# Optimization experiments

Measured on AMD Instinct MI355X. Metric: run time of the kernel, lower is better.

The kernel has to match this reference:

```python
import jax, jax.numpy as jnp
import numpy as np

B, T, C = 128, 512, 128  # batch, seq_len, num_tags


def setup_inputs() -> dict:
    key = jax.random.key(0)
    k1, k2, k3 = jax.random.split(key, 3)
    labels = jax.random.randint(k1, (B, T), 0, C)
    y_true = jax.nn.one_hot(labels, C, dtype=jnp.float32)  # dense one-hot targets
    y_pred = jax.random.normal(k2, (B, T, C), dtype=jnp.float32)  # emission scores
    mask = jnp.ones((B, T), dtype=jnp.float32)
    # glorot_uniform for (C,C): limit = sqrt(6/(C+C))
    limit = np.sqrt(6.0 / (C + C)).astype(np.float32)
    trans = jax.random.uniform(k3, (C, C), dtype=jnp.float32, minval=-limit, maxval=limit)
    return {"y_true": y_true, "y_pred": y_pred, "mask": mask, "trans": trans}


def reference(y_true, y_pred, mask, trans):
    # Faithful translation of ConditionalRandomField.dense_loss (lr_multiplier=1).
    m = mask[..., None]                      # (B,T,1)
    y_true = y_true * m
    y_pred = y_pred * m
    # real path score
    emission = jnp.einsum('bnc,bnc->b', y_true, y_pred)
    transition = jnp.einsum('bni,ij,bnj->b', y_true[:, :-1], trans, y_true[:, 1:])
    real_path_score = emission + transition  # (B,)
    # forward algorithm: sequential logsumexp recurrence (K.rnn equivalent)
    init = y_pred[:, 0]                      # (B,C)
    xs = (jnp.swapaxes(y_pred[:, 1:], 0, 1),  # (T-1,B,C)
          jnp.swapaxes(mask[:, 1:], 0, 1))    # (T-1,B)

    def step(state, xm):
        x_t, m_t = xm
        # state: (B,C) alpha; trans: (C,C)
        new = jax.nn.logsumexp(state[:, :, None] + trans[None, :, :], axis=1) + x_t
        state = jnp.where(m_t[:, None] > 0, new, state)  # masked steps carry prev state
        return state, None

    last, _ = jax.lax.scan(step, init, xs)
    all_paths_score = jax.nn.logsumexp(last, axis=1)  # (B,)
    return all_paths_score - real_path_score          # (B,) per-sample CRF NLL
```

## Files before the change

kernel.cpp:

```cpp
#include <hip/hip_runtime.h>

#define BB 128
#define TT 512
#define CC 128

typedef short short8 __attribute__((ext_vector_type(8)));
typedef float f32x4  __attribute__((ext_vector_type(4)));
typedef unsigned u32x4 __attribute__((ext_vector_type(4)));

__device__ __forceinline__ unsigned pk_trunc(float a, float b) {
    return __builtin_amdgcn_perm(__float_as_uint(a), __float_as_uint(b), 0x03020706u);
}
__device__ __forceinline__ unsigned short f2bf(float f) {
    unsigned u = __float_as_uint(f);
    u += 0x7fffu + ((u >> 16) & 1u);
    return (unsigned short)(u >> 16);
}
__device__ __forceinline__ float lo16f(unsigned u) { return __uint_as_float(u << 16); }
__device__ __forceinline__ float hi16f(unsigned u) { return __uint_as_float(u & 0xffff0000u); }

#define MFMA16(A, B, C) __builtin_amdgcn_mfma_f32_16x16x32_bf16((A), (B), (C), 0, 0, 0)

#define DOSTEP(AP_, P_, RPAR_, TN_) do {                                       \
    const unsigned* sb = &sbuf[RPAR_][0];                                      \
    unsigned* sw = &sbuf[(RPAR_) ^ 1][0];                                      \
    u32x4 Rv1 = *(const u32x4*)(sb + rd1);                                     \
    u32x4 Rv2 = *(const u32x4*)(sb + rd2);                                     \
    u32x4 Rv3 = *(const u32x4*)(sb + rd3);                                     \
    unsigned bcu = 0;                                                          \
    if (AP_) bcu = sb[bcaddr];                    \
    const float mm = pfm[P_];                                                  \
    float e0[4], e1[4];                                                        \
    e0[0] = __expf(pfa[P_].x * mm); e0[1] = __expf(pfa[P_].y * mm);            \
    e0[2] = __expf(pfa[P_].z * mm); e0[3] = __expf(pfa[P_].w * mm);            \
    e1[0] = __expf(pfb[P_].x * mm); e1[1] = __expf(pfb[P_].y * mm);            \
    e1[2] = __expf(pfb[P_].z * mm); e1[3] = __expf(pfb[P_].w * mm);            \
    union { u32x4 u; short8 s; } cO, c1, c2, c3;                               \
    cO.u[0] = BfO[0]; cO.u[1] = BfO[1]; cO.u[2] = BfO[2]; cO.u[3] = BfO[3];    \
    c1.u = Rv1; c2.u = Rv2; c3.u = Rv3;                                        \
    f32x4 aA0 = {0.f,0.f,0.f,0.f}, aA1 = {0.f,0.f,0.f,0.f};                    \
    f32x4 aB0 = {0.f,0.f,0.f,0.f}, aB1 = {0.f,0.f,0.f,0.f};                    \
    aA0 = MFMA16(AfP[0][0], cO.s, aA0);  aA1 = MFMA16(AfP[1][0], cO.s, aA1);   \
    aA0 = MFMA16(AfP[0][1], c1.s, aA0);  aA1 = MFMA16(AfP[1][1], c1.s, aA1);   \
    aB0 = MFMA16(AfP[0][2], c2.s, aB0);  aB1 = MFMA16(AfP[1][2], c2.s, aB1);   \
    aB0 = MFMA16(AfP[0][3], c3.s, aB0);  aB1 = MFMA16(AfP[1][3], c3.s, aB1);   \
    f32x4 ac0 = aA0 + aB0, ac1 = aA1 + aB1;                                    \
    float pend = 1.f;                                                          \
    if (AP_) {                                                                 \
        float bc = lo16f(bcu);                                                 \
        pend = __builtin_amdgcn_rcpf(bc);                                      \
        lacc += __logf(bc);                                                    \
    }                                                                          \
    float v00 = ac0[0]*e0[0], v01 = ac0[1]*e0[1];                              \
    float v02 = ac0[2]*e0[2], v03 = ac0[3]*e0[3];                              \
    float v10 = ac1[0]*e1[0], v11 = ac1[1]*e1[1];                              \
    float v12 = ac1[2]*e1[2], v13 = ac1[3]*e1[3];                              \
    if (AP_) {                                                                 \
        v00 *= pend; v01 *= pend; v02 *= pend; v03 *= pend;                    \
        v10 *= pend; v11 *= pend; v12 *= pend; v13 *= pend;                    \
    }                                                                          \
    unsigned n0 = pk_trunc(v00, v01), n1 = pk_trunc(v02, v03);                 \
    unsigned n2 = pk_trunc(v10, v11), n3 = pk_trunc(v12, v13);                 \
    if (__ballot(mm <= 0.f)) {                  \
        unsigned k0 = pk_trunc(lo16f(BfO[0]) * pend, hi16f(BfO[0]) * pend);    \
        unsigned k1 = pk_trunc(lo16f(BfO[1]) * pend, hi16f(BfO[1]) * pend);    \
        unsigned k2 = pk_trunc(lo16f(BfO[2]) * pend, hi16f(BfO[2]) * pend);    \
        unsigned k3 = pk_trunc(lo16f(BfO[3]) * pend, hi16f(BfO[3]) * pend);    \
        const bool kk = (mm <= 0.f);                                           \
        n0 = kk ? k0 : n0; n1 = kk ? k1 : n1;                                  \
        n2 = kk ? k2 : n2; n3 = kk ? k3 : n3;                                  \
    }                                                                          \
    u32x4 wv; wv[0] = n0; wv[1] = n1; wv[2] = n2; wv[3] = n3;                  \
    *(u32x4*)(sw + wwOwn) = wv;                   \
    BfO[0] = n0; BfO[1] = n1; BfO[2] = n2; BfO[3] = n3;                        \
    if ((TN_) >= 0) {                                  \
        pfa[P_] = *(const float4*)(yb + (size_t)(TN_) * CC + ch0p);            \
        pfb[P_] = *(const float4*)(yb + (size_t)(TN_) * CC + ch0p + 4);        \
        pfm[P_] = mrow[TN_];                                                   \
    }                                                                          \
    asm volatile("s_waitcnt lgkmcnt(0)" ::: "memory");                         \
    __builtin_amdgcn_s_barrier();                 \
    asm volatile("" ::: "memory");                                             \
} while (0)

__global__ __launch_bounds__(256, 1) void crf_all(
    const float* __restrict__ y_true, const float* __restrict__ y_pred,
    const float* __restrict__ mask, const float* __restrict__ trans,
    float* __restrict__ out)
{
    __shared__ __align__(16) unsigned sbuf[2][1024];
    __shared__ float red[4][16];

    const int tid  = threadIdx.x;
    const int lane = tid & 63;
    const int w    = tid >> 6;

    if (blockIdx.x >= 8) {
        const int rb  = blockIdx.x - 8;
        const int ts  = w * 128;
        const int te  = min(ts + 128, TT - 1);
        const float* yt_b = y_true + (size_t)rb * TT * CC;
        const float* yp_b = y_pred + (size_t)rb * TT * CC;
        const float* m_b  = mask + (size_t)rb * TT;

        float em = 0.f, tr = 0.f;
        int lprev = 0; float mprev = 0.f;
        const float* ytr = yt_b + ts * CC;
        const float* ypr = yp_b + ts * CC;
        float cyt0 = ytr[lane], cyt1 = ytr[lane + 64];
        float cyp0 = ypr[lane], cyp1 = ypr[lane + 64];
        float cm = m_b[ts];
        for (int t = ts; t <= te; ++t) {
            float nyt0 = 0.f, nyt1 = 0.f, nyp0 = 0.f, nyp1 = 0.f, nm = 0.f;
            if (t < te) {
                const float* ytn = yt_b + (t + 1) * CC;
                const float* ypn = yp_b + (t + 1) * CC;
                nyt0 = ytn[lane]; nyt1 = ytn[lane + 64];
                nyp0 = ypn[lane]; nyp1 = ypn[lane + 64];
                nm = m_b[t + 1];
            }
            unsigned long long b0 = __ballot(cyt0 > 0.5f);
            unsigned long long b1 = __ballot(cyt1 > 0.5f);
            int l = b0 ? (__ffsll(b0) - 1) : (64 + __ffsll(b1) - 1);
            float v0 = __shfl(cyp0, l & 63);
            float v1 = __shfl(cyp1, l & 63);
            float v  = (l < 64) ? v0 : v1;
            if (lane == 0) {
                if (t < ts + 128) em += cm * cm * v;
                if (t > ts)       tr += mprev * cm * trans[lprev * CC + l];
            }
            lprev = l; mprev = cm;
            cyt0 = nyt0; cyt1 = nyt1; cyp0 = nyp0; cyp1 = nyp1; cm = nm;
        }
        if (lane == 0) atomicAdd(&out[rb], -(em + tr));
        return;
    }

    const int bq = lane & 15;
    const int q  = lane >> 4;
    const int g  = blockIdx.x;
    const float* yb   = y_pred + (size_t)(g * 16 + bq) * TT * CC;
    const float* mrow = mask + (size_t)(g * 16 + bq) * TT;
    const int ch0p = 32 * w + 8 * q;

    const float4 i0 = *(const float4*)(yb + ch0p);
    const float4 i1 = *(const float4*)(yb + ch0p + 4);
    const float  m0 = mrow[0];
    float4 pfa[4], pfb[4]; float pfm[4];
    #pragma unroll
    for (int p = 0; p < 4; ++p) {
        pfa[p] = *(const float4*)(yb + (size_t)(1 + p) * CC + ch0p);
        pfb[p] = *(const float4*)(yb + (size_t)(1 + p) * CC + ch0p + 4);
        pfm[p] = mrow[1 + p];
    }

    short8 AfP[2][4];
    #pragma unroll
    for (int n2 = 0; n2 < 2; ++n2) {
        const int j = 32 * w + 8 * (bq >> 2) + 4 * n2 + (bq & 3);
        #pragma unroll
        for (int i = 0; i < 4; ++i) {
            const int kt = (w + i) & 3;
            #pragma unroll
            for (int e = 0; e < 8; ++e)
                AfP[n2][i][e] = (short)f2bf(__expf(trans[(kt * 32 + q * 8 + e) * CC + j]));
        }
    }

    const int swz = (bq & 7) << 2;
    const int rd1 = bq * 64 + ((((w + 1) & 3) * 16 + 4 * q) ^ swz);
    const int rd2 = bq * 64 + ((((w + 2) & 3) * 16 + 4 * q) ^ swz);
    const int rd3 = bq * 64 + ((((w + 3) & 3) * 16 + 4 * q) ^ swz);
    const int wwOwn = bq * 64 + ((16 * w + 4 * q) ^ swz);
    const int bcaddr = bq * 64 + swz;

    unsigned BfO[4];

    {
        unsigned n0 = pk_trunc(__expf(i0.x * m0), __expf(i0.y * m0));
        unsigned n1 = pk_trunc(__expf(i0.z * m0), __expf(i0.w * m0));
        unsigned n2 = pk_trunc(__expf(i1.x * m0), __expf(i1.y * m0));
        unsigned n3 = pk_trunc(__expf(i1.z * m0), __expf(i1.w * m0));
        u32x4 wv; wv[0] = n0; wv[1] = n1; wv[2] = n2; wv[3] = n3;
        *(u32x4*)(&sbuf[0][0] + wwOwn) = wv;
        BfO[0] = n0; BfO[1] = n1; BfO[2] = n2; BfO[3] = n3;
    }
    asm volatile("s_waitcnt lgkmcnt(0)" ::: "memory");
    __builtin_amdgcn_s_barrier();
    asm volatile("" ::: "memory");

    float lacc = 0.f;

    for (int tt = 1; tt <= 505; tt += 4) {
        int t4 = tt + 4, t5 = tt + 5, t6 = tt + 6, t7 = tt + 7;
        if (t7 > TT - 1) t7 = TT - 1;
        DOSTEP(true,  0, 0, t4);
        DOSTEP(false, 1, 1, t5);
        DOSTEP(false, 2, 0, t6);
        DOSTEP(false, 3, 1, t7);
    }
    DOSTEP(true,  0, 0, -1);
    DOSTEP(false, 1, 1, -1);

    {
        const unsigned* sb = &sbuf[0][0];
        u32x4 Rv1 = *(const u32x4*)(sb + rd1);
        u32x4 Rv2 = *(const u32x4*)(sb + rd2);
        u32x4 Rv3 = *(const u32x4*)(sb + rd3);
        const float mm = pfm[2];
        float e0[4], e1[4];
        e0[0] = __expf(pfa[2].x * mm); e0[1] = __expf(pfa[2].y * mm);
        e0[2] = __expf(pfa[2].z * mm); e0[3] = __expf(pfa[2].w * mm);
        e1[0] = __expf(pfb[2].x * mm); e1[1] = __expf(pfb[2].y * mm);
        e1[2] = __expf(pfb[2].z * mm); e1[3] = __expf(pfb[2].w * mm);
        union { u32x4 u; short8 s; } cO, c1, c2, c3;
        cO.u[0] = BfO[0]; cO.u[1] = BfO[1]; cO.u[2] = BfO[2]; cO.u[3] = BfO[3];
        c1.u = Rv1; c2.u = Rv2; c3.u = Rv3;
        f32x4 aA0 = {0.f,0.f,0.f,0.f}, aA1 = {0.f,0.f,0.f,0.f};
        f32x4 aB0 = {0.f,0.f,0.f,0.f}, aB1 = {0.f,0.f,0.f,0.f};
        aA0 = MFMA16(AfP[0][0], cO.s, aA0);  aA1 = MFMA16(AfP[1][0], cO.s, aA1);
        aA0 = MFMA16(AfP[0][1], c1.s, aA0);  aA1 = MFMA16(AfP[1][1], c1.s, aA1);
        aB0 = MFMA16(AfP[0][2], c2.s, aB0);  aB1 = MFMA16(AfP[1][2], c2.s, aB1);
        aB0 = MFMA16(AfP[0][3], c3.s, aB0);  aB1 = MFMA16(AfP[1][3], c3.s, aB1);
        f32x4 ac0 = aA0 + aB0, ac1 = aA1 + aB1;
        float ssum = ac0[0]*e0[0] + ac0[1]*e0[1] + ac0[2]*e0[2] + ac0[3]*e0[3]
                   + ac1[0]*e1[0] + ac1[1]*e1[1] + ac1[2]*e1[2] + ac1[3]*e1[3];
        if (__ballot(mm <= 0.f)) {
            float os = lo16f(BfO[0]) + hi16f(BfO[0]) + lo16f(BfO[1]) + hi16f(BfO[1])
                     + lo16f(BfO[2]) + hi16f(BfO[2]) + lo16f(BfO[3]) + hi16f(BfO[3]);
            ssum = (mm <= 0.f) ? os : ssum;
        }
        ssum += __shfl_xor(ssum, 16, 64);
        ssum += __shfl_xor(ssum, 32, 64);
        if (lane < 16) red[w][lane] = ssum;
        asm volatile("s_waitcnt lgkmcnt(0)" ::: "memory");
        __builtin_amdgcn_s_barrier();
        asm volatile("" ::: "memory");
        if (w == 0 && lane < 16) {
            float tot = red[0][lane] + red[1][lane] + red[2][lane] + red[3][lane];
            atomicAdd(&out[g * 16 + lane], __logf(tot) + lacc);
        }
    }
}

extern "C" void kernel_launch(void* const* d_in, const int* in_sizes, int n_in,
                              void* d_out, int out_size, void* d_ws, size_t ws_size,
                              hipStream_t stream) {
    (void)in_sizes; (void)n_in; (void)out_size; (void)d_ws; (void)ws_size;
    const float* y_true = (const float*)d_in[0];
    const float* y_pred = (const float*)d_in[1];
    const float* mask   = (const float*)d_in[2];
    const float* trans  = (const float*)d_in[3];
    float* out = (float*)d_out;

    hipMemsetAsync(out, 0, BB * sizeof(float), stream);
    crf_all<<<dim3(8 + BB), 256, 0, stream>>>(y_true, y_pred, mask, trans, out);
}
```

Baseline: 253.3 us.

## Interleave two batch groups per block in forward recurrence to hide latency

Each forward-recurrence block now handles two independent 16-sample groups (4 blocks instead of 8), interleaving their MFMA chains, exponentials and LDS traffic inside each step. This gives the latency-bound serial recurrence independent work to fill pipeline stalls and halves the number of per-step barriers per sample. Exponentials switch to exp2f with a pre-scaled LOG2E factor. The cost is more registers and LDS per block, and only 4 CUs now run the critical serial path, so per-step work doubles on each of them.

```diff
diff --git a/kernel.cpp b/kernel.cpp
--- a/kernel.cpp
+++ b/kernel.cpp
@@ -20,63 +20,106 @@
 __device__ __forceinline__ float hi16f(unsigned u) { return __uint_as_float(u & 0xffff0000u); }
 
 #define MFMA16(A, B, C) __builtin_amdgcn_mfma_f32_16x16x32_bf16((A), (B), (C), 0, 0, 0)
-
-#define DOSTEP(AP_, P_, RPAR_, TN_) do {                                       \
-    const unsigned* sb = &sbuf[RPAR_][0];                                      \
-    unsigned* sw = &sbuf[(RPAR_) ^ 1][0];                                      \
-    u32x4 Rv1 = *(const u32x4*)(sb + rd1);                                     \
-    u32x4 Rv2 = *(const u32x4*)(sb + rd2);                                     \
-    u32x4 Rv3 = *(const u32x4*)(sb + rd3);                                     \
-    unsigned bcu = 0;                                                          \
-    if (AP_) bcu = sb[bcaddr];                    \
-    const float mm = pfm[P_];                                                  \
-    float e0[4], e1[4];                                                        \
-    e0[0] = __expf(pfa[P_].x * mm); e0[1] = __expf(pfa[P_].y * mm);            \
-    e0[2] = __expf(pfa[P_].z * mm); e0[3] = __expf(pfa[P_].w * mm);            \
-    e1[0] = __expf(pfb[P_].x * mm); e1[1] = __expf(pfb[P_].y * mm);            \
-    e1[2] = __expf(pfb[P_].z * mm); e1[3] = __expf(pfb[P_].w * mm);            \
-    union { u32x4 u; short8 s; } cO, c1, c2, c3;                               \
-    cO.u[0] = BfO[0]; cO.u[1] = BfO[1]; cO.u[2] = BfO[2]; cO.u[3] = BfO[3];    \
-    c1.u = Rv1; c2.u = Rv2; c3.u = Rv3;                                        \
-    f32x4 aA0 = {0.f,0.f,0.f,0.f}, aA1 = {0.f,0.f,0.f,0.f};                    \
-    f32x4 aB0 = {0.f,0.f,0.f,0.f}, aB1 = {0.f,0.f,0.f,0.f};                    \
-    aA0 = MFMA16(AfP[0][0], cO.s, aA0);  aA1 = MFMA16(AfP[1][0], cO.s, aA1);   \
-    aA0 = MFMA16(AfP[0][1], c1.s, aA0);  aA1 = MFMA16(AfP[1][1], c1.s, aA1);   \
-    aB0 = MFMA16(AfP[0][2], c2.s, aB0);  aB1 = MFMA16(AfP[1][2], c2.s, aB1);   \
-    aB0 = MFMA16(AfP[0][3], c3.s, aB0);  aB1 = MFMA16(AfP[1][3], c3.s, aB1);   \
+#define LOG2E 1.442695041f
+
+#define DOSTEP2(AP_, P_, RPAR_, TN_) do {                                      \
+    const unsigned* sb0 = &sbuf[0][RPAR_][0];                                  \
+    unsigned* sw0 = &sbuf[0][(RPAR_) ^ 1][0];                                  \
+    const unsigned* sb1 = &sbuf[1][RPAR_][0];                                  \
+    unsigned* sw1 = &sbuf[1][(RPAR_) ^ 1][0];                                  \
+    u32x4 Rva1 = *(const u32x4*)(sb0 + rd1);                                   \
+    u32x4 Rva2 = *(const u32x4*)(sb0 + rd2);                                   \
+    u32x4 Rva3 = *(const u32x4*)(sb0 + rd3);                                   \
+    u32x4 Rvb1 = *(const u32x4*)(sb1 + rd1);                                   \
+    u32x4 Rvb2 = *(const u32x4*)(sb1 + rd2);                                   \
+    u32x4 Rvb3 = *(const u32x4*)(sb1 + rd3);                                   \
+    unsigned bcu0 = 0, bcu1 = 0;                                               \
+    if (AP_) { bcu0 = sb0[bcaddr]; bcu1 = sb1[bcaddr]; }                       \
+    const float mm0 = pfm0[P_], mm1 = pfm1[P_];                                \
+    const float mL0 = mm0 * LOG2E, mL1 = mm1 * LOG2E;                          \
+    float ea0[4], ea1[4], eb0[4], eb1[4];                                      \
+    ea0[0] = exp2f(pfa0[P_].x * mL0); ea0[1] = exp2f(pfa0[P_].y * mL0);        \
+    ea0[2] = exp2f(pfa0[P_].z * mL0); ea0[3] = exp2f(pfa0[P_].w * mL0);        \
+    ea1[0] = exp2f(pfb0[P_].x * mL0); ea1[1] = exp2f(pfb0[P_].y * mL0);        \
+    ea1[2] = exp2f(pfb0[P_].z * mL0); ea1[3] = exp2f(pfb0[P_].w * mL0);        \
+    eb0[0] = exp2f(pfa1[P_].x * mL1); eb0[1] = exp2f(pfa1[P_].y * mL1);        \
+    eb0[2] = exp2f(pfa1[P_].z * mL1); eb0[3] = exp2f(pfa1[P_].w * mL1);        \
+    eb1[0] = exp2f(pfb1[P_].x * mL1); eb1[1] = exp2f(pfb1[P_].y * mL1);        \
+    eb1[2] = exp2f(pfb1[P_].z * mL1); eb1[3] = exp2f(pfb1[P_].w * mL1);        \
+    union { u32x4 u; short8 s; } cOa, ca1, ca2, ca3, cOb, cb1, cb2, cb3;       \
+    cOa.u[0] = BfO0[0]; cOa.u[1] = BfO0[1];                                    \
+    cOa.u[2] = BfO0[2]; cOa.u[3] = BfO0[3];                                    \
+    cOb.u[0] = BfO1[0]; cOb.u[1] = BfO1[1];                                    \
+    cOb.u[2] = BfO1[2]; cOb.u[3] = BfO1[3];                                    \
+    ca1.u = Rva1; ca2.u = Rva2; ca3.u = Rva3;                                  \
+    cb1.u = Rvb1; cb2.u = Rvb2; cb3.u = Rvb3;                                  \
+    f32x4 aA0, aA1, aB0, aB1, bA0, bA1, bB0, bB1;                              \
+    aA0 = MFMA16(AfP[0][0], cOa.s, Z4);  aA1 = MFMA16(AfP[1][0], cOa.s, Z4);   \
+    bA0 = MFMA16(AfP[0][0], cOb.s, Z4);  bA1 = MFMA16(AfP[1][0], cOb.s, Z4);   \
+    aA0 = MFMA16(AfP[0][1], ca1.s, aA0); aA1 = MFMA16(AfP[1][1], ca1.s, aA1);  \
+    bA0 = MFMA16(AfP[0][1], cb1.s, bA0); bA1 = MFMA16(AfP[1][1], cb1.s, bA1);  \
+    aB0 = MFMA16(AfP[0][2], ca2.s, Z4);  aB1 = MFMA16(AfP[1][2], ca2.s, Z4);   \
+    bB0 = MFMA16(AfP[0][2], cb2.s, Z4);  bB1 = MFMA16(AfP[1][2], cb2.s, Z4);   \
+    aB0 = MFMA16(AfP[0][3], ca3.s, aB0); aB1 = MFMA16(AfP[1][3], ca3.s, aB1);  \
+    bB0 = MFMA16(AfP[0][3], cb3.s, bB0); bB1 = MFMA16(AfP[1][3], cb3.s, bB1);  \
     f32x4 ac0 = aA0 + aB0, ac1 = aA1 + aB1;                                    \
-    float pend = 1.f;                                                          \
+    f32x4 bc0 = bA0 + bB0, bc1 = bA1 + bB1;                                    \
+    float pend0 = 1.f, pend1 = 1.f;                                            \
     if (AP_) {                                                                 \
-        float bc = lo16f(bcu);                                                 \
-        pend = __builtin_amdgcn_rcpf(bc);                                      \
-        lacc += __logf(bc);                                                    \
-    }                                                                          \
-    float v00 = ac0[0]*e0[0], v01 = ac0[1]*e0[1];                              \
-    float v02 = ac0[2]*e0[2], v03 = ac0[3]*e0[3];                              \
-    float v10 = ac1[0]*e1[0], v11 = ac1[1]*e1[1];                              \
-    float v12 = ac1[2]*e1[2], v13 = ac1[3]*e1[3];                              \
+        float v0_ = lo16f(bcu0), v1_ = lo16f(bcu1);                            \
+        pend0 = __builtin_amdgcn_rcpf(v0_);                                    \
+        pend1 = __builtin_amdgcn_rcpf(v1_);                                    \
+        lacc0 += __logf(v0_); lacc1 += __logf(v1_);                            \
+    }                                                                          \
+    float v00 = ac0[0]*ea0[0], v01 = ac0[1]*ea0[1];                            \
+    float v02 = ac0[2]*ea0[2], v03 = ac0[3]*ea0[3];                            \
+    float v10 = ac1[0]*ea1[0], v11 = ac1[1]*ea1[1];                            \
+    float v12 = ac1[2]*ea1[2], v13 = ac1[3]*ea1[3];                            \
+    float w00 = bc0[0]*eb0[0], w01 = bc0[1]*eb0[1];                            \
+    float w02 = bc0[2]*eb0[2], w03 = bc0[3]*eb0[3];                            \
+    float w10 = bc1[0]*eb1[0], w11 = bc1[1]*eb1[1];                            \
+    float w12 = bc1[2]*eb1[2], w13 = bc1[3]*eb1[3];                            \
     if (AP_) {                                                                 \
-        v00 *= pend; v01 *= pend; v02 *= pend; v03 *= pend;                    \
-        v10 *= pend; v11 *= pend; v12 *= pend; v13 *= pend;                    \
+        v00 *= pend0; v01 *= pend0; v02 *= pend0; v03 *= pend0;                \
+        v10 *= pend0; v11 *= pend0; v12 *= pend0; v13 *= pend0;                \
+        w00 *= pend1; w01 *= pend1; w02 *= pend1; w03 *= pend1;                \
+        w10 *= pend1; w11 *= pend1; w12 *= pend1; w13 *= pend1;                \
     }                                                                          \
     unsigned n0 = pk_trunc(v00, v01), n1 = pk_trunc(v02, v03);                 \
     unsigned n2 = pk_trunc(v10, v11), n3 = pk_trunc(v12, v13);                 \
-    if (__ballot(mm <= 0.f)) {                  \
-        unsigned k0 = pk_trunc(lo16f(BfO[0]) * pend, hi16f(BfO[0]) * pend);    \
-        unsigned k1 = pk_trunc(lo16f(BfO[1]) * pend, hi16f(BfO[1]) * pend);    \
-        unsigned k2 = pk_trunc(lo16f(BfO[2]) * pend, hi16f(BfO[2]) * pend);    \
-        unsigned k3 = pk_trunc(lo16f(BfO[3]) * pend, hi16f(BfO[3]) * pend);    \
-        const bool kk = (mm <= 0.f);                                           \
+    unsigned m0_ = pk_trunc(w00, w01), m1_ = pk_trunc(w02, w03);               \
+    unsigned m2_ = pk_trunc(w10, w11), m3_ = pk_trunc(w12, w13);               \
+    if (__ballot(mm0 <= 0.f)) {                 \
+        unsigned k0 = pk_trunc(lo16f(BfO0[0]) * pend0, hi16f(BfO0[0]) * pend0);\
+        unsigned k1 = pk_trunc(lo16f(BfO0[1]) * pend0, hi16f(BfO0[1]) * pend0);\
+        unsigned k2 = pk_trunc(lo16f(BfO0[2]) * pend0, hi16f(BfO0[2]) * pend0);\
+        unsigned k3 = pk_trunc(lo16f(BfO0[3]) * pend0, hi16f(BfO0[3]) * pend0);\
+        const bool kk = (mm0 <= 0.f);                                          \
         n0 = kk ? k0 : n0; n1 = kk ? k1 : n1;                                  \
         n2 = kk ? k2 : n2; n3 = kk ? k3 : n3;                                  \
     }                                                                          \
-    u32x4 wv; wv[0] = n0; wv[1] = n1; wv[2] = n2; wv[3] = n3;                  \
-    *(u32x4*)(sw + wwOwn) = wv;                   \
-    BfO[0] = n0; BfO[1] = n1; BfO[2] = n2; BfO[3] = n3;                        \
-    if ((TN_) >= 0) {                                  \
-        pfa[P_] = *(const float4*)(yb + (size_t)(TN_) * CC + ch0p);            \
-        pfb[P_] = *(const float4*)(yb + (size_t)(TN_) * CC + ch0p + 4);        \
-        pfm[P_] = mrow[TN_];                                                   \
+    if (__ballot(mm1 <= 0.f)) {                                                \
+        unsigned k0 = pk_trunc(lo16f(BfO1[0]) * pend1, hi16f(BfO1[0]) * pend1);\
+        unsigned k1 = pk_trunc(lo16f(BfO1[1]) * pend1, hi16f(BfO1[1]) * pend1);\
+        unsigned k2 = pk_trunc(lo16f(BfO1[2]) * pend1, hi16f(BfO1[2]) * pend1);\
+        unsigned k3 = pk_trunc(lo16f(BfO1[3]) * pend1, hi16f(BfO1[3]) * pend1);\
+        const bool kk = (mm1 <= 0.f);                                          \
+        m0_ = kk ? k0 : m0_; m1_ = kk ? k1 : m1_;                              \
+        m2_ = kk ? k2 : m2_; m3_ = kk ? k3 : m3_;                              \
+    }                                                                          \
+    u32x4 wva; wva[0] = n0;  wva[1] = n1;  wva[2] = n2;  wva[3] = n3;          \
+    u32x4 wvb; wvb[0] = m0_; wvb[1] = m1_; wvb[2] = m2_; wvb[3] = m3_;         \
+    *(u32x4*)(sw0 + wwOwn) = wva;                                              \
+    *(u32x4*)(sw1 + wwOwn) = wvb;                                              \
+    BfO0[0] = n0;  BfO0[1] = n1;  BfO0[2] = n2;  BfO0[3] = n3;                 \
+    BfO1[0] = m0_; BfO1[1] = m1_; BfO1[2] = m2_; BfO1[3] = m3_;                \
+    if ((TN_) >= 0) {                            \
+        pfa0[P_] = *(const float4*)(yb0 + (size_t)(TN_) * CC + ch0p);          \
+        pfb0[P_] = *(const float4*)(yb0 + (size_t)(TN_) * CC + ch0p + 4);      \
+        pfm0[P_] = mrow0[TN_];                                                 \
+        pfa1[P_] = *(const float4*)(yb1 + (size_t)(TN_) * CC + ch0p);          \
+        pfb1[P_] = *(const float4*)(yb1 + (size_t)(TN_) * CC + ch0p + 4);      \
+        pfm1[P_] = mrow1[TN_];                                                 \
     }                                                                          \
     asm volatile("s_waitcnt lgkmcnt(0)" ::: "memory");                         \
     __builtin_amdgcn_s_barrier();                 \
@@ -88,15 +131,15 @@
     const float* __restrict__ mask, const float* __restrict__ trans,
     float* __restrict__ out)
 {
-    __shared__ __align__(16) unsigned sbuf[2][1024];
-    __shared__ float red[4][16];
+    __shared__ __align__(16) unsigned sbuf[2][2][1024];
+    __shared__ float red[2][4][16];
 
     const int tid  = threadIdx.x;
     const int lane = tid & 63;
     const int w    = tid >> 6;
 
-    if (blockIdx.x >= 8) {
-        const int rb  = blockIdx.x - 8;
+    if (blockIdx.x >= 4) {
+        const int rb  = blockIdx.x - 4;
         const int ts  = w * 128;
         const int te  = min(ts + 128, TT - 1);
         const float* yt_b = y_true + (size_t)rb * TT * CC;
@@ -138,20 +181,28 @@
 
     const int bq = lane & 15;
     const int q  = lane >> 4;
-    const int g  = blockIdx.x;
-    const float* yb   = y_pred + (size_t)(g * 16 + bq) * TT * CC;
-    const float* mrow = mask + (size_t)(g * 16 + bq) * TT;
+    const int g0 = blockIdx.x * 2;
+    const int g1 = g0 + 1;
+    const float* yb0   = y_pred + (size_t)(g0 * 16 + bq) * TT * CC;
+    const float* yb1   = y_pred + (size_t)(g1 * 16 + bq) * TT * CC;
+    const float* mrow0 = mask + (size_t)(g0 * 16 + bq) * TT;
+    const float* mrow1 = mask + (size_t)(g1 * 16 + bq) * TT;
     const int ch0p = 32 * w + 8 * q;
 
-    const float4 i0 = *(const float4*)(yb + ch0p);
-    const float4 i1 = *(const float4*)(yb + ch0p + 4);
-    const float  m0 = mrow[0];
-    float4 pfa[4], pfb[4]; float pfm[4];
+    const float4 i00 = *(const float4*)(yb0 + ch0p);
+    const float4 i01 = *(const float4*)(yb0 + ch0p + 4);
+    const float4 i10 = *(const float4*)(yb1 + ch0p);
+    const float4 i11 = *(const float4*)(yb1 + ch0p + 4);
+    const float  m00 = mrow0[0], m10 = mrow1[0];
+    float4 pfa0[4], pfb0[4], pfa1[4], pfb1[4]; float pfm0[4], pfm1[4];
     #pragma unroll
     for (int p = 0; p < 4; ++p) {
-        pfa[p] = *(const float4*)(yb + (size_t)(1 + p) * CC + ch0p);
-        pfb[p] = *(const float4*)(yb + (size_t)(1 + p) * CC + ch0p + 4);
-        pfm[p] = mrow[1 + p];
+        pfa0[p] = *(const float4*)(yb0 + (size_t)(1 + p) * CC + ch0p);
+        pfb0[p] = *(const float4*)(yb0 + (size_t)(1 + p) * CC + ch0p + 4);
+        pfm0[p] = mrow0[1 + p];
+        pfa1[p] = *(const float4*)(yb1 + (size_t)(1 + p) * CC + ch0p);
+        pfb1[p] = *(const float4*)(yb1 + (size_t)(1 + p) * CC + ch0p + 4);
+        pfm1[p] = mrow1[1 + p];
     }
 
     short8 AfP[2][4];
@@ -174,53 +225,65 @@
     const int wwOwn = bq * 64 + ((16 * w + 4 * q) ^ swz);
     const int bcaddr = bq * 64 + swz;
 
-    unsigned BfO[4];
+    const f32x4 Z4 = {0.f, 0.f, 0.f, 0.f};
+    unsigned BfO0[4], BfO1[4];
 
     {
-        unsigned n0 = pk_trunc(__expf(i0.x * m0), __expf(i0.y * m0));
-        unsigned n1 = pk_trunc(__expf(i0.z * m0), __expf(i0.w * m0));
-        unsigned n2 = pk_trunc(__expf(i1.x * m0), __expf(i1.y * m0));
-        unsigned n3 = pk_trunc(__expf(i1.z * m0), __expf(i1.w * m0));
+        unsigned n0 = pk_trunc(__expf(i00.x * m00), __expf(i00.y * m00));
+        unsigned n1 = pk_trunc(__expf(i00.z * m00), __expf(i00.w * m00));
+        unsigned n2 = pk_trunc(__expf(i01.x * m00), __expf(i01.y * m00));
+        unsigned n3 = pk_trunc(__expf(i01.z * m00), __expf(i01.w * m00));
         u32x4 wv; wv[0] = n0; wv[1] = n1; wv[2] = n2; wv[3] = n3;
-        *(u32x4*)(&sbuf[0][0] + wwOwn) = wv;
-        BfO[0] = n0; BfO[1] = n1; BfO[2] = n2; BfO[3] = n3;
+        *(u32x4*)(&sbuf[0][0][0] + wwOwn) = wv;
+        BfO0[0] = n0; BfO0[1] = n1; BfO0[2] = n2; BfO0[3] = n3;
+        unsigned p0 = pk_trunc(__expf(i10.x * m10), __expf(i10.y * m10));
+        unsigned p1 = pk_trunc(__expf(i10.z * m10), __expf(i10.w * m10));
+        unsigned p2 = pk_trunc(__expf(i11.x * m10), __expf(i11.y * m10));
+        unsigned p3 = pk_trunc(__expf(i11.z * m10), __expf(i11.w * m10));
+        u32x4 wv2; wv2[0] = p0; wv2[1] = p1; wv2[2] = p2; wv2[3] = p3;
+        *(u32x4*)(&sbuf[1][0][0] + wwOwn) = wv2;
+        BfO1[0] = p0; BfO1[1] = p1; BfO1[2] = p2; BfO1[3] = p3;
     }
     asm volatile("s_waitcnt lgkmcnt(0)" ::: "memory");
     __builtin_amdgcn_s_barrier();
     asm volatile("" ::: "memory");
 
-    float lacc = 0.f;
+    float lacc0 = 0.f, lacc1 = 0.f;
 
     for (int tt = 1; tt <= 505; tt += 4) {
         int t4 = tt + 4, t5 = tt + 5, t6 = tt + 6, t7 = tt + 7;
         if (t7 > TT - 1) t7 = TT - 1;
-        DOSTEP(true,  0, 0, t4);
-        DOSTEP(false, 1, 1, t5);
-        DOSTEP(false, 2, 0, t6);
-        DOSTEP(false, 3, 1, t7);
-    }
-    DOSTEP(true,  0, 0, -1);
-    DOSTEP(false, 1, 1, -1);
-
-    {
-        const unsigned* sb = &sbuf[0][0];
+        DOSTEP2(true,  0, 0, t4);
+        DOSTEP2(false, 1, 1, t5);
+        DOSTEP2(false, 2, 0, t6);
+        DOSTEP2(false, 3, 1, t7);
+    }
+    DOSTEP2(true,  0, 0, -1);
+    DOSTEP2(false, 1, 1, -1);
+
+    #pragma unroll
+    for (int h = 0; h < 2; ++h) {
+        const unsigned* sb = &sbuf[h][0][0];
         u32x4 Rv1 = *(const u32x4*)(sb + rd1);
         u32x4 Rv2 = *(const u32x4*)(sb + rd2);
         u32x4 Rv3 = *(const u32x4*)(sb + rd3);
-        const float mm = pfm[2];
+        const float mm = h ? pfm1[2] : pfm0[2];
+        const float4 va = h ? pfa1[2] : pfa0[2];
+        const float4 vb = h ? pfb1[2] : pfb0[2];
+        const unsigned* BfO = h ? BfO1 : BfO0;
+        const float mL = mm * LOG2E;
         float e0[4], e1[4];
-        e0[0] = __expf(pfa[2].x * mm); e0[1] = __expf(pfa[2].y * mm);
-        e0[2] = __expf(pfa[2].z * mm); e0[3] = __expf(pfa[2].w * mm);
-        e1[0] = __expf(pfb[2].x * mm); e1[1] = __expf(pfb[2].y * mm);
-        e1[2] = __expf(pfb[2].z * mm); e1[3] = __expf(pfb[2].w * mm);
+        e0[0] = exp2f(va.x * mL); e0[1] = exp2f(va.y * mL);
+        e0[2] = exp2f(va.z * mL); e0[3] = exp2f(va.w * mL);
+        e1[0] = exp2f(vb.x * mL); e1[1] = exp2f(vb.y * mL);
+        e1[2] = exp2f(vb.z * mL); e1[3] = exp2f(vb.w * mL);
         union { u32x4 u; short8 s; } cO, c1, c2, c3;
         cO.u[0] = BfO[0]; cO.u[1] = BfO[1]; cO.u[2] = BfO[2]; cO.u[3] = BfO[3];
         c1.u = Rv1; c2.u = Rv2; c3.u = Rv3;
-        f32x4 aA0 = {0.f,0.f,0.f,0.f}, aA1 = {0.f,0.f,0.f,0.f};
-        f32x4 aB0 = {0.f,0.f,0.f,0.f}, aB1 = {0.f,0.f,0.f,0.f};
-        aA0 = MFMA16(AfP[0][0], cO.s, aA0);  aA1 = MFMA16(AfP[1][0], cO.s, aA1);
+        f32x4 aA0, aA1, aB0, aB1;
+        aA0 = MFMA16(AfP[0][0], cO.s, Z4);   aA1 = MFMA16(AfP[1][0], cO.s, Z4);
         aA0 = MFMA16(AfP[0][1], c1.s, aA0);  aA1 = MFMA16(AfP[1][1], c1.s, aA1);
-        aB0 = MFMA16(AfP[0][2], c2.s, aB0);  aB1 = MFMA16(AfP[1][2], c2.s, aB1);
+        aB0 = MFMA16(AfP[0][2], c2.s, Z4);   aB1 = MFMA16(AfP[1][2], c2.s, Z4);
         aB0 = MFMA16(AfP[0][3], c3.s, aB0);  aB1 = MFMA16(AfP[1][3], c3.s, aB1);
         f32x4 ac0 = aA0 + aB0, ac1 = aA1 + aB1;
         float ssum = ac0[0]*e0[0] + ac0[1]*e0[1] + ac0[2]*e0[2] + ac0[3]*e0[3]
@@ -232,14 +295,18 @@
         }
         ssum += __shfl_xor(ssum, 16, 64);
         ssum += __shfl_xor(ssum, 32, 64);
-        if (lane < 16) red[w][lane] = ssum;
-        asm volatile("s_waitcnt lgkmcnt(0)" ::: "memory");
-        __builtin_amdgcn_s_barrier();
-        asm volatile("" ::: "memory");
-        if (w == 0 && lane < 16) {
-            float tot = red[0][lane] + red[1][lane] + red[2][lane] + red[3][lane];
-            atomicAdd(&out[g * 16 + lane], __logf(tot) + lacc);
-        }
+        if (lane < 16) red[h][w][lane] = ssum;
+    }
+    asm volatile("s_waitcnt lgkmcnt(0)" ::: "memory");
+    __builtin_amdgcn_s_barrier();
+    asm volatile("" ::: "memory");
+    if (w == 0 && lane < 16) {
+        float tot0 = red[0][0][lane] + red[0][1][lane]
+                   + red[0][2][lane] + red[0][3][lane];
+        float tot1 = red[1][0][lane] + red[1][1][lane]
+                   + red[1][2][lane] + red[1][3][lane];
+        atomicAdd(&out[g0 * 16 + lane], __logf(tot0) + lacc0);
+        atomicAdd(&out[g1 * 16 + lane], __logf(tot1) + lacc1);
     }
 }
 
@@ -254,5 +321,5 @@
     float* out = (float*)d_out;
 
     hipMemsetAsync(out, 0, BB * sizeof(float), stream);
-    crf_all<<<dim3(8 + BB), 256, 0, stream>>>(y_true, y_pred, mask, trans, out);
+    crf_all<<<dim3(4 + BB), 256, 0, stream>>>(y_true, y_pred, mask, trans, out);
 }
```

New measurement: 443.5 us. +75.1%, slower.
